# Kernel tuning notes

Hardware: AMD Instinct MI355X
Metric: run time of the kernel (lower is better)

The kernel has to match this reference:

```python
import jax, jax.numpy as jnp
import numpy as np

N = 50000      # nodes
E = 640000     # edges
F = 128        # input features
NHID = 128
HEAD = 4
DH = NHID // HEAD
NUM_SCATTER = 3
LAYER = 2
G = 256        # graphs in batch
C = 10         # classes
EPS = 1e-5


def setup_inputs() -> dict:
    key = jax.random.key(0)
    k = jax.random.split(key, 20)
    s = 1.0 / np.sqrt(NHID)
    return {
        "x": jax.random.normal(k[0], (N, F), jnp.float32),
        "edge_attr": jax.random.uniform(k[1], (E,), jnp.float32),
        "lin_w": jax.random.normal(k[2], (F, NHID), jnp.float32) / np.sqrt(F),
        "lin_b": jnp.zeros((NHID,), jnp.float32),
        "conv_W": jax.random.normal(k[3], (NUM_SCATTER, LAYER, NHID, NHID), jnp.float32) * s,
        "conv_asrc": jax.random.normal(k[4], (NUM_SCATTER, LAYER, HEAD, DH), jnp.float32) * s,
        "conv_adst": jax.random.normal(k[5], (NUM_SCATTER, LAYER, HEAD, DH), jnp.float32) * s,
        "fc_w1": jax.random.normal(k[6], (NHID, 64), jnp.float32) * s,
        "fc_b1": jnp.zeros((64,), jnp.float32),
        "bn_g1": jnp.ones((64,), jnp.float32),
        "bn_b1": jnp.zeros((64,), jnp.float32),
        "fc_w2": jax.random.normal(k[7], (64, 32), jnp.float32) / np.sqrt(64.0),
        "fc_b2": jnp.zeros((32,), jnp.float32),
        "bn_g2": jnp.ones((32,), jnp.float32),
        "bn_b2": jnp.zeros((32,), jnp.float32),
        "fc_w3": jax.random.normal(k[8], (32, C), jnp.float32) / np.sqrt(32.0),
        "fc_b3": jnp.zeros((C,), jnp.float32),
        "bn_g3": jnp.ones((C,), jnp.float32),
        "bn_b3": jnp.zeros((C,), jnp.float32),
        "edge_index": jax.random.randint(k[9], (2, E), 0, N, jnp.int32),
        "batch": jnp.sort(jax.random.randint(k[10], (N,), 0, G, jnp.int32)),
    }


def _batchnorm(z, g, b):
    m = z.mean(0)
    v = z.var(0)
    return (z - m) * jax.lax.rsqrt(v + EPS) * g + b


def _scatter_conv(h, W, asrc, adst, src, dst, edge_attr):
    # GAT-like Scatter block with LAYER inner layers, HEAD attention heads.
    for l in range(LAYER):
        wx = (h @ W[l]).reshape(N, HEAD, DH)                 # [N,H,Dh]
        a_s = jnp.einsum("nhd,hd->nh", wx, asrc[l])          # [N,H]
        a_d = jnp.einsum("nhd,hd->nh", wx, adst[l])
        e = jax.nn.leaky_relu(a_s[src] + a_d[dst], 0.2) * edge_attr[:, None]  # [E,H]
        # destination-segment softmax
        e_max = jax.ops.segment_max(e, dst, num_segments=N)
        e_exp = jnp.exp(e - e_max[dst])
        denom = jax.ops.segment_sum(e_exp, dst, num_segments=N)
        alpha = e_exp / (denom[dst] + 1e-16)                 # [E,H]
        msg = alpha[:, :, None] * wx[src]                    # [E,H,Dh]
        agg = jax.ops.segment_sum(msg, dst, num_segments=N).reshape(N, NHID)
        h = jax.nn.elu(agg)
    return h


def reference(x, edge_attr, lin_w, lin_b, conv_W, conv_asrc, conv_adst,
              fc_w1, fc_b1, bn_g1, bn_b1, fc_w2, fc_b2, bn_g2, bn_b2,
              fc_w3, fc_b3, bn_g3, bn_b3, edge_index, batch):
    src, dst = edge_index[0], edge_index[1]
    h = x @ lin_w + lin_b                                    # lin_in
    for i in range(NUM_SCATTER):                             # residual scatter convs
        h = h + _scatter_conv(h, conv_W[i], conv_asrc[i], conv_adst[i], src, dst, edge_attr)
    pooled = jax.ops.segment_sum(h, batch, num_segments=G)   # global_add_pool [G,NHID]
    z = jax.nn.relu(_batchnorm(pooled @ fc_w1 + fc_b1, bn_g1, bn_b1))
    z = jax.nn.relu(_batchnorm(z @ fc_w2 + fc_b2, bn_g2, bn_b2))
    z = _batchnorm(z @ fc_w3 + fc_b3, bn_g3, bn_b3)          # final Linear+BN, no relu
    return z
```

## Files before the change

### kernel.cpp

```cpp
#include <hip/hip_runtime.h>
#include <hip/hip_fp16.h>
#include <math.h>

#define N_NODES 50000
#define N_EDGES 640000
#define NGRAPH  256
#define NBUCK   196
#define EPB     8192
#define NBLK    79
#define BCAP    6144

#define PB_HIST  NBLK
#define PB_WPREP 448
#define PB_APREP 48
#define PB_ZERO  128
#define PREP_GRID (PB_HIST + PB_WPREP + PB_APREP + PB_ZERO)

typedef _Float16 half8_t __attribute__((ext_vector_type(8)));
typedef float floatx4 __attribute__((ext_vector_type(4)));

__global__ __launch_bounds__(256) void k_prep(
    const int* __restrict__ dst, int* __restrict__ counts,
    const float* __restrict__ lin_w, const float* __restrict__ conv_W,
    _Float16* __restrict__ wt_g,
    const float* __restrict__ conv_asrc, const float* __restrict__ conv_adst,
    _Float16* __restrict__ aux_g,
    float* __restrict__ pooled)
{
    __shared__ int h[256];
    int b = blockIdx.x;
    if (b < PB_HIST) {
        h[threadIdx.x] = 0;
        __syncthreads();
        int e0 = b * EPB;
        int e1 = e0 + EPB; if (e1 > N_EDGES) e1 = N_EDGES;
        for (int e = e0 + threadIdx.x; e < e1; e += 256)
            atomicAdd(&h[dst[e] >> 8], 1);
        __syncthreads();
        counts[b * 256 + threadIdx.x] = h[threadIdx.x];
    } else if (b < PB_HIST + PB_WPREP) {
        int idx = (b - PB_HIST) * 256 + threadIdx.x;
        int m = idx >> 14;
        int r = idx & 16383;
        int k = r >> 7;
        int n = r & 127;
        const float* W = (m == 0) ? lin_w : conv_W + (size_t)(m - 1) * 16384;
        float v = W[(size_t)k * 128 + n];
        int slot = (k >> 3) ^ (n & 15);
        wt_g[(size_t)m * 16384 + n * 128 + slot * 8 + (k & 7)] = (_Float16)v;
    } else if (b < PB_HIST + PB_WPREP + PB_APREP) {
        int idx = (b - PB_HIST - PB_WPREP) * 256 + threadIdx.x;
        int li = idx >> 11;
        int r = idx & 2047;
        int k = r >> 4;
        int n = r & 15;
        float v = 0.f;
        if (n < 8) {
            int hh = n & 3;
            const float* a = (n < 4) ? conv_asrc : conv_adst;
            const float* Wrow = conv_W + (size_t)li * 16384 + (size_t)k * 128 + hh * 32;
            const float* av = a + (size_t)li * 128 + hh * 32;
            #pragma unroll 8
            for (int d = 0; d < 32; ++d) v += Wrow[d] * av[d];
        }
        int slot = (k >> 3) ^ n;
        aux_g[(size_t)li * 2048 + n * 128 + slot * 8 + (k & 7)] = (_Float16)v;
    } else {
        int idx = (b - PB_HIST - PB_WPREP - PB_APREP) * 256 + threadIdx.x;
        pooled[idx] = 0.f;
    }
}

template <bool AF32>
__global__ __launch_bounds__(256) void k_gemm16(
    const void* __restrict__ Av, const _Float16* __restrict__ wt,
    const _Float16* __restrict__ aux, const float* __restrict__ bias,
    __half* __restrict__ C16, int M,
    float* __restrict__ a_s, float* __restrict__ a_d)
{
    __shared__ _Float16 Wt[128 * 128];
    __shared__ _Float16 Waux[16 * 128];
    int tid = threadIdx.x;
    {
        const float4* wsrc = (const float4*)wt;
        float4* wl = (float4*)Wt;
        #pragma unroll
        for (int r = 0; r < 8; ++r) wl[r * 256 + tid] = wsrc[r * 256 + tid];
        if (aux) ((float4*)Waux)[tid] = ((const float4*)aux)[tid];
    }
    __syncthreads();

    int lane = tid & 63;
    int wv = tid >> 6;
    int r0 = blockIdx.x * 64 + wv * 16;
    int cl = lane & 15;
    int ks = lane >> 4;

    int arow = r0 + cl; if (arow >= M) arow = M - 1;
    half8_t afrag[4];
    if (AF32) {
        const float* ArowF = (const float*)Av + (size_t)arow * 128 + ks * 8;
        #pragma unroll
        for (int kk = 0; kk < 4; ++kk) {
            float4 f0 = *(const float4*)(ArowF + kk * 32);
            float4 f1 = *(const float4*)(ArowF + kk * 32 + 4);
            half8_t a;
            a[0] = (_Float16)f0.x; a[1] = (_Float16)f0.y;
            a[2] = (_Float16)f0.z; a[3] = (_Float16)f0.w;
            a[4] = (_Float16)f1.x; a[5] = (_Float16)f1.y;
            a[6] = (_Float16)f1.z; a[7] = (_Float16)f1.w;
            afrag[kk] = a;
        }
    } else {
        const _Float16* Arow = (const _Float16*)Av + (size_t)arow * 128 + ks * 8;
        #pragma unroll
        for (int kk = 0; kk < 4; ++kk)
            afrag[kk] = *(const half8_t*)(Arow + kk * 32);
    }

    floatx4 acc[8];
    #pragma unroll
    for (int nt = 0; nt < 8; ++nt) acc[nt] = (floatx4){0.f, 0.f, 0.f, 0.f};

    #pragma unroll
    for (int kk = 0; kk < 4; ++kk) {
        #pragma unroll
        for (int nt = 0; nt < 8; ++nt) {
            int n = nt * 16 + cl;
            int slot = (kk * 4 + ks) ^ cl;
            half8_t bfrag = *(const half8_t*)&Wt[n * 128 + slot * 8];
            acc[nt] = __builtin_amdgcn_mfma_f32_16x16x32_f16(afrag[kk], bfrag, acc[nt], 0, 0, 0);
        }
    }

    int rg = lane >> 4;
    #pragma unroll
    for (int nt = 0; nt < 8; ++nt) {
        float bv = bias ? bias[nt * 16 + cl] : 0.f;
        #pragma unroll
        for (int j = 0; j < 4; ++j) {
            int row = r0 + rg * 4 + j;
            if (row < M)
                C16[(size_t)row * 128 + nt * 16 + cl] = __float2half(acc[nt][j] + bv);
        }
    }

    if (a_s) {
        floatx4 accP = (floatx4){0.f, 0.f, 0.f, 0.f};
        #pragma unroll
        for (int kk = 0; kk < 4; ++kk) {
            int slot = (kk * 4 + ks) ^ cl;
            half8_t bfrag = *(const half8_t*)&Waux[cl * 128 + slot * 8];
            accP = __builtin_amdgcn_mfma_f32_16x16x32_f16(afrag[kk], bfrag, accP, 0, 0, 0);
        }
        if (cl < 8) {
            float* dstp = (cl < 4) ? a_s : a_d;
            int h = cl & 3;
            #pragma unroll
            for (int j = 0; j < 4; ++j) {
                int row = r0 + rg * 4 + j;
                if (row < M) dstp[row * 4 + h] = accP[j];
            }
        }
    }
}

__global__ __launch_bounds__(256) void k_scan2(const int* __restrict__ counts,
                                               int* __restrict__ base,
                                               int* __restrict__ bucketBase)
{
    __shared__ int tot[256];
    __shared__ int pref[257];
    int b = threadIdx.x;
    int s = 0;
    for (int blk = 0; blk < NBLK; ++blk) s += counts[blk * 256 + b];
    tot[b] = s;
    __syncthreads();
    if (b == 0) {
        int run = 0;
        for (int i = 0; i < 256; ++i) { pref[i] = run; run += tot[i]; }
        pref[256] = run;
    }
    __syncthreads();
    if (b <= NBUCK) bucketBase[b] = pref[b];
    int run = pref[b];
    for (int blk = 0; blk < NBLK; ++blk) {
        base[blk * 256 + b] = run;
        run += counts[blk * 256 + b];
    }
}

__global__ __launch_bounds__(256) void k_bin(const int* __restrict__ src,
                                             const int* __restrict__ dst,
                                             const float* __restrict__ ea,
                                             const int* __restrict__ base,
                                             int2* __restrict__ binned)
{
    __shared__ int cur[256];
    cur[threadIdx.x] = base[blockIdx.x * 256 + threadIdx.x];
    __syncthreads();
    int e0 = blockIdx.x * EPB;
    int e1 = e0 + EPB; if (e1 > N_EDGES) e1 = N_EDGES;
    for (int e = e0 + threadIdx.x; e < e1; e += 256) {
        int d = dst[e];
        int p = atomicAdd(&cur[d >> 8], 1);
        binned[p] = make_int2(src[e] | ((d & 255) << 16), __float_as_int(ea[e]));
    }
}

__global__ __launch_bounds__(256) void k_sortfill(const int2* __restrict__ binned,
                                                  const int* __restrict__ bucketBase,
                                                  int2* __restrict__ edata,
                                                  int* __restrict__ offs)
{
    __shared__ int bx[BCAP];
    __shared__ int by[BCAP];
    __shared__ int cnt[256];
    __shared__ int nb[256];
    int b = blockIdx.x;
    int p0 = bucketBase[b], p1 = bucketBase[b + 1];
    int m = p1 - p0;
    if (m > BCAP) m = BCAP;
    cnt[threadIdx.x] = 0;
    __syncthreads();
    for (int i = threadIdx.x; i < m; i += 256) {
        int2 v = binned[p0 + i];
        bx[i] = v.x; by[i] = v.y;
        atomicAdd(&cnt[(v.x >> 16) & 255], 1);
    }
    __syncthreads();
    if (threadIdx.x == 0) {
        int run = 0;
        for (int i = 0; i < 256; ++i) { nb[i] = run; run += cnt[i]; }
    }
    __syncthreads();
    int node = b * 256 + threadIdx.x;
    if (node < N_NODES) offs[node] = p0 + nb[threadIdx.x];
    if (b == NBUCK - 1 && threadIdx.x == 0) offs[N_NODES] = p1;
    __syncthreads();
    cnt[threadIdx.x] = nb[threadIdx.x];
    __syncthreads();
    for (int i = threadIdx.x; i < m; i += 256) {
        int dl = (bx[i] >> 16) & 255;
        int pos = atomicAdd(&cnt[dl], 1);
        edata[p0 + pos] = make_int2(bx[i] & 0xFFFF, by[i]);
    }
}

__global__ __launch_bounds__(256) void k_attn5(
    const __half* __restrict__ wx16, const int2* __restrict__ edata,
    const float* __restrict__ a_s, const float* __restrict__ a_d,
    const int* __restrict__ offs, const __half* __restrict__ resid,
    __half* __restrict__ out)
{
    int lane = threadIdx.x & 63;
    int wid = threadIdx.x >> 6;
    int nh = lane >> 5;
    int n = blockIdx.x * 8 + wid * 2 + nh;
    int q = (lane >> 2) & 7;
    int cl = lane & 3;
    int c0 = cl * 32;
    int ht = cl;
    int off0 = offs[n], off1 = offs[n + 1];
    int cnt = off1 - off0;
    float adn = a_d[n * 4 + ht];
    const _Float16* wx = (const _Float16*)wx16;

    float den = 0.f;
    float acc[32];
    #pragma unroll
    for (int k = 0; k < 32; ++k) acc[k] = 0.f;

    #define STEP(jj) {                                                         \
        int2 ed = edata[off0 + (jj)];                                          \
        float t = a_s[ed.x * 4 + ht] + adn;                                    \
        t = (t > 0.f ? t : 0.2f * t) * __int_as_float(ed.y);                   \
        float w = __expf(fminf(t, 80.f));                                      \
        den += w;                                                              \
        const _Float16* rp = &wx[(size_t)ed.x * 128 + c0];                     \
        half8_t g0 = *(const half8_t*)rp;                                      \
        half8_t g1 = *(const half8_t*)(rp + 8);                                \
        half8_t g2 = *(const half8_t*)(rp + 16);                               \
        half8_t g3 = *(const half8_t*)(rp + 24);                               \
        _Pragma("unroll")                                                      \
        for (int k = 0; k < 8; ++k) {                                          \
            acc[k]      += w * (float)g0[k];                                   \
            acc[8 + k]  += w * (float)g1[k];                                   \
            acc[16 + k] += w * (float)g2[k];                                   \
            acc[24 + k] += w * (float)g3[k];                                   \
        } }

    int j = q;
    for (; j + 8 < cnt; j += 16) { STEP(j); STEP(j + 8); }
    if (j < cnt) STEP(j);
    #undef STEP

    den += __shfl_xor(den, 4);
    den += __shfl_xor(den, 8);
    den += __shfl_xor(den, 16);
    #pragma unroll
    for (int k = 0; k < 32; ++k) {
        acc[k] += __shfl_xor(acc[k], 4);
        acc[k] += __shfl_xor(acc[k], 8);
        acc[k] += __shfl_xor(acc[k], 16);
    }

    if (q == 0) {
        float inv = 1.f / (den + 1e-16f);
        const _Float16* rvp = resid ? (const _Float16*)resid + (size_t)n * 128 + c0 : nullptr;
        _Float16* op = (_Float16*)out + (size_t)n * 128 + c0;
        #pragma unroll
        for (int v = 0; v < 4; ++v) {
            half8_t rv;
            if (resid) rv = *(const half8_t*)(rvp + v * 8);
            half8_t o;
            #pragma unroll
            for (int k = 0; k < 8; ++k) {
                float r = acc[v * 8 + k] * inv;
                r = r > 0.f ? r : (__expf(r) - 1.f);
                if (resid) r += (float)rv[k];
                o[k] = (_Float16)r;
            }
            *(half8_t*)(op + v * 8) = o;
        }
    }
}

__global__ __launch_bounds__(256) void k_pool2(
    const __half* __restrict__ h, const int* __restrict__ batch,
    float* __restrict__ pooled)
{
    int c = threadIdx.x & 127;
    int hf = threadIdx.x >> 7;
    int n0 = blockIdx.x * 64 + hf * 32;
    if (n0 >= N_NODES) return;
    int nend = n0 + 32; if (nend > N_NODES) nend = N_NODES;

    int g = batch[n0];
    float acc = 0.f;
    for (int n = n0; n < nend; ++n) {
        int bg = batch[n];
        if (bg != g) { atomicAdd(&pooled[g * 128 + c], acc); acc = 0.f; g = bg; }
        acc += __half2float(h[(size_t)n * 128 + c]);
    }
    atomicAdd(&pooled[g * 128 + c], acc);
}

template <int K, int OC>
__global__ __launch_bounds__(256) void k_mlp(
    const float* __restrict__ in, const float* __restrict__ w,
    const float* __restrict__ b, const float* __restrict__ gam,
    const float* __restrict__ bet, float* __restrict__ out, int do_relu)
{
    __shared__ float2 red[256];
    int c = blockIdx.x, g = threadIdx.x;
    float val = b[c];
    #pragma unroll 8
    for (int k = 0; k < K; ++k) val += in[g * K + k] * w[k * OC + c];
    red[g] = make_float2(val, val * val);
    __syncthreads();
    for (int s = 128; s > 0; s >>= 1) {
        if (g < s) { red[g].x += red[g + s].x; red[g].y += red[g + s].y; }
        __syncthreads();
    }
    float mean = red[0].x * (1.f / 256.f);
    float var = red[0].y * (1.f / 256.f) - mean * mean;
    float y = (val - mean) * rsqrtf(var + 1e-5f) * gam[c] + bet[c];
    if (do_relu) y = fmaxf(y, 0.f);
    out[g * OC + c] = y;
}

extern "C" void kernel_launch(void* const* d_in, const int* in_sizes, int n_in,
                              void* d_out, int out_size, void* d_ws, size_t ws_size,
                              hipStream_t stream)
{
    const float* x         = (const float*)d_in[0];
    const float* edge_attr = (const float*)d_in[1];
    const float* lin_w     = (const float*)d_in[2];
    const float* lin_b     = (const float*)d_in[3];
    const float* conv_W    = (const float*)d_in[4];
    const float* conv_asrc = (const float*)d_in[5];
    const float* conv_adst = (const float*)d_in[6];
    const float* fc_w1 = (const float*)d_in[7];
    const float* fc_b1 = (const float*)d_in[8];
    const float* bn_g1 = (const float*)d_in[9];
    const float* bn_b1 = (const float*)d_in[10];
    const float* fc_w2 = (const float*)d_in[11];
    const float* fc_b2 = (const float*)d_in[12];
    const float* bn_g2 = (const float*)d_in[13];
    const float* bn_b2 = (const float*)d_in[14];
    const float* fc_w3 = (const float*)d_in[15];
    const float* fc_b3 = (const float*)d_in[16];
    const float* bn_g3 = (const float*)d_in[17];
    const float* bn_b3 = (const float*)d_in[18];
    const int* edge_index = (const int*)d_in[19];
    const int* batch      = (const int*)d_in[20];
    const int* srcp = edge_index;
    const int* dstp = edge_index + N_EDGES;
    float* out = (float*)d_out;

    char* ws = (char*)d_ws;
    __half* h_cur = (__half*)ws; ws += (size_t)N_NODES * 128 * 2;
    __half* h_tmp = (__half*)ws; ws += (size_t)N_NODES * 128 * 2;
    __half* wx16  = (__half*)ws; ws += (size_t)N_NODES * 128 * 2;
    float* a_s   = (float*)ws;  ws += (size_t)N_NODES * 4 * 4;
    float* a_d   = (float*)ws;  ws += (size_t)N_NODES * 4 * 4;
    float* pooled= (float*)ws;  ws += (size_t)NGRAPH * 128 * 4;
    float* z1    = (float*)ws;  ws += (size_t)NGRAPH * 64 * 4;
    float* z2    = (float*)ws;  ws += (size_t)NGRAPH * 32 * 4;
    int* offs    = (int*)ws;    ws += (size_t)(N_NODES + 4) * 4;
    int2* edata  = (int2*)ws;   ws += (size_t)N_EDGES * 8;
    int2* binned = (int2*)ws;   ws += (size_t)N_EDGES * 8;
    int* counts  = (int*)ws;    ws += (size_t)NBLK * 256 * 4;
    int* base    = (int*)ws;    ws += (size_t)NBLK * 256 * 4;
    int* bucketBase = (int*)ws; ws += 256 * 4;
    _Float16* wt_g = (_Float16*)ws; ws += (size_t)7 * 16384 * 2;
    _Float16* wt_aux = (_Float16*)ws; ws += (size_t)6 * 2048 * 2;

    k_prep<<<PREP_GRID, 256, 0, stream>>>(dstp, counts, lin_w, conv_W, wt_g,
                                          conv_asrc, conv_adst, wt_aux, pooled);
    k_scan2<<<1, 256, 0, stream>>>(counts, base, bucketBase);
    k_bin<<<NBLK, 256, 0, stream>>>(srcp, dstp, edge_attr, base, binned);
    k_sortfill<<<NBUCK, 256, 0, stream>>>(binned, bucketBase, edata, offs);

    const int GGRID = (N_NODES + 63) / 64;
    const int AGRID = (N_NODES + 7) / 8;

    k_gemm16<true><<<GGRID, 256, 0, stream>>>(x, wt_g, nullptr, lin_b, h_cur,
                                              N_NODES, nullptr, nullptr);

    for (int i = 0; i < 3; ++i) {
        const _Float16* W0 = wt_g + (size_t)(1 + i * 2 + 0) * 16384;
        const _Float16* W1 = wt_g + (size_t)(1 + i * 2 + 1) * 16384;
        const _Float16* X0 = wt_aux + (size_t)(i * 2 + 0) * 2048;
        const _Float16* X1 = wt_aux + (size_t)(i * 2 + 1) * 2048;

        k_gemm16<false><<<GGRID, 256, 0, stream>>>(h_cur, W0, X0, nullptr, wx16,
                                                   N_NODES, a_s, a_d);
        k_attn5<<<AGRID, 256, 0, stream>>>(wx16, edata, a_s, a_d,
                                           offs, nullptr, h_tmp);

        k_gemm16<false><<<GGRID, 256, 0, stream>>>(h_tmp, W1, X1, nullptr, wx16,
                                                   N_NODES, a_s, a_d);
        k_attn5<<<AGRID, 256, 0, stream>>>(wx16, edata, a_s, a_d,
                                           offs, h_cur, h_cur);
    }

    k_pool2<<<GGRID, 256, 0, stream>>>(h_cur, batch, pooled);
    k_mlp<128, 64><<<64, 256, 0, stream>>>(pooled, fc_w1, fc_b1, bn_g1, bn_b1, z1, 1);
    k_mlp<64, 32><<<32, 256, 0, stream>>>(z1, fc_w2, fc_b2, bn_g2, bn_b2, z2, 1);
    k_mlp<32, 10><<<10, 256, 0, stream>>>(z2, fc_w3, fc_b3, bn_g3, bn_b3, out, 0);
}
```

Baseline: 462.7 us.

## Split attention aggregation by head across four blocks to cut register use

The edge-attention aggregation kernel now launches four times as many blocks, one per attention head. Each thread accumulates 8 feature channels instead of 32, which shrinks the accumulator array and the shuffle reduction and should raise occupancy for the latency-bound gather. In exchange, edge indices, attention scores and the exp are recomputed four times per edge (once per head-block). Each row gather becomes a narrower 16-byte load per lane.

```diff
diff --git a/kernel.cpp b/kernel.cpp
--- a/kernel.cpp
+++ b/kernel.cpp
@@ -247,48 +247,42 @@
     }
 }
 
-__global__ __launch_bounds__(256) void k_attn5(
+__global__ __launch_bounds__(256) void k_attn6(
     const __half* __restrict__ wx16, const int2* __restrict__ edata,
     const float* __restrict__ a_s, const float* __restrict__ a_d,
     const int* __restrict__ offs, const __half* __restrict__ resid,
     __half* __restrict__ out)
 {
+    int line = blockIdx.x & 3;
+    int ng = blockIdx.x >> 2;
     int lane = threadIdx.x & 63;
     int wid = threadIdx.x >> 6;
     int nh = lane >> 5;
-    int n = blockIdx.x * 8 + wid * 2 + nh;
+    int n = ng * 8 + wid * 2 + nh;
     int q = (lane >> 2) & 7;
     int cl = lane & 3;
-    int c0 = cl * 32;
-    int ht = cl;
+    int c0 = line * 32 + cl * 8;
     int off0 = offs[n], off1 = offs[n + 1];
     int cnt = off1 - off0;
-    float adn = a_d[n * 4 + ht];
+    float adn = a_d[n * 4 + line];
     const _Float16* wx = (const _Float16*)wx16;
 
     float den = 0.f;
-    float acc[32];
+    float acc[8];
     #pragma unroll
-    for (int k = 0; k < 32; ++k) acc[k] = 0.f;
+    for (int k = 0; k < 8; ++k) acc[k] = 0.f;
 
     #define STEP(jj) {                                                         \
         int2 ed = edata[off0 + (jj)];                                          \
-        float t = a_s[ed.x * 4 + ht] + adn;                                    \
+        float t = a_s[ed.x * 4 + line] + adn;                                  \
         t = (t > 0.f ? t : 0.2f * t) * __int_as_float(ed.y);                   \
         float w = __expf(fminf(t, 80.f));                                      \
         den += w;                                                              \
-        const _Float16* rp = &wx[(size_t)ed.x * 128 + c0];                     \
-        half8_t g0 = *(const half8_t*)rp;                                      \
-        half8_t g1 = *(const half8_t*)(rp + 8);                                \
-        half8_t g2 = *(const half8_t*)(rp + 16);                               \
-        half8_t g3 = *(const half8_t*)(rp + 24);                               \
-        _Pragma("unroll")                                                      \
-        for (int k = 0; k < 8; ++k) {                                          \
-            acc[k]      += w * (float)g0[k];                                   \
-            acc[8 + k]  += w * (float)g1[k];                                   \
-            acc[16 + k] += w * (float)g2[k];                                   \
-            acc[24 + k] += w * (float)g3[k];                                   \
-        } }
+        half8_t g = *(const half8_t*)&wx[(size_t)ed.x * 128 + c0];             \
+        acc[0] += w * (float)g[0]; acc[1] += w * (float)g[1];                  \
+        acc[2] += w * (float)g[2]; acc[3] += w * (float)g[3];                  \
+        acc[4] += w * (float)g[4]; acc[5] += w * (float)g[5];                  \
+        acc[6] += w * (float)g[6]; acc[7] += w * (float)g[7]; }
 
     int j = q;
     for (; j + 8 < cnt; j += 16) { STEP(j); STEP(j + 8); }
@@ -299,7 +293,7 @@
     den += __shfl_xor(den, 8);
     den += __shfl_xor(den, 16);
     #pragma unroll
-    for (int k = 0; k < 32; ++k) {
+    for (int k = 0; k < 8; ++k) {
         acc[k] += __shfl_xor(acc[k], 4);
         acc[k] += __shfl_xor(acc[k], 8);
         acc[k] += __shfl_xor(acc[k], 16);
@@ -307,22 +301,17 @@
 
     if (q == 0) {
         float inv = 1.f / (den + 1e-16f);
-        const _Float16* rvp = resid ? (const _Float16*)resid + (size_t)n * 128 + c0 : nullptr;
-        _Float16* op = (_Float16*)out + (size_t)n * 128 + c0;
-        #pragma unroll
-        for (int v = 0; v < 4; ++v) {
-            half8_t rv;
-            if (resid) rv = *(const half8_t*)(rvp + v * 8);
-            half8_t o;
-            #pragma unroll
-            for (int k = 0; k < 8; ++k) {
-                float r = acc[v * 8 + k] * inv;
-                r = r > 0.f ? r : (__expf(r) - 1.f);
-                if (resid) r += (float)rv[k];
-                o[k] = (_Float16)r;
-            }
-            *(half8_t*)(op + v * 8) = o;
-        }
+        half8_t rv;
+        if (resid) rv = *(const half8_t*)((const _Float16*)resid + (size_t)n * 128 + c0);
+        half8_t o;
+        #pragma unroll
+        for (int k = 0; k < 8; ++k) {
+            float r = acc[k] * inv;
+            r = r > 0.f ? r : (__expf(r) - 1.f);
+            if (resid) r += (float)rv[k];
+            o[k] = (_Float16)r;
+        }
+        *(half8_t*)((_Float16*)out + (size_t)n * 128 + c0) = o;
     }
 }
 
@@ -424,7 +413,7 @@
     k_sortfill<<<NBUCK, 256, 0, stream>>>(binned, bucketBase, edata, offs);
 
     const int GGRID = (N_NODES + 63) / 64;
-    const int AGRID = (N_NODES + 7) / 8;
+    const int AGRID = ((N_NODES + 7) / 8) * 4;
 
     k_gemm16<true><<<GGRID, 256, 0, stream>>>(x, wt_g, nullptr, lin_b, h_cur,
                                               N_NODES, nullptr, nullptr);
@@ -437,16 +426,16 @@
 
         k_gemm16<false><<<GGRID, 256, 0, stream>>>(h_cur, W0, X0, nullptr, wx16,
                                                    N_NODES, a_s, a_d);
-        k_attn5<<<AGRID, 256, 0, stream>>>(wx16, edata, a_s, a_d,
+        k_attn6<<<AGRID, 256, 0, stream>>>(wx16, edata, a_s, a_d,
                                            offs, nullptr, h_tmp);
 
         k_gemm16<false><<<GGRID, 256, 0, stream>>>(h_tmp, W1, X1, nullptr, wx16,
                                                    N_NODES, a_s, a_d);
-        k_attn5<<<AGRID, 256, 0, stream>>>(wx16, edata, a_s, a_d,
+        k_attn6<<<AGRID, 256, 0, stream>>>(wx16, edata, a_s, a_d,
                                            offs, h_cur, h_cur);
     }
 
-    k_pool2<<<GGRID, 256, 0, stream>>>(h_cur, batch, pooled);
+    k_pool2<<<(N_NODES + 63) / 64, 256, 0, stream>>>(h_cur, batch, pooled);
     k_mlp<128, 64><<<64, 256, 0, stream>>>(pooled, fc_w1, fc_b1, bn_g1, bn_b1, z1, 1);
     k_mlp<64, 32><<<32, 256, 0, stream>>>(z1, fc_w2, fc_b2, bn_g2, bn_b2, z2, 1);
     k_mlp<32, 10><<<10, 256, 0, stream>>>(z2, fc_w3, fc_b3, bn_g3, bn_b3, out, 0);
```

Measured after the change: 511.1 us. +10.4%, slower.
